# Kernel optimization log

Measured on AMD Instinct MI355X. Metric: run time of the kernel, lower is better.

The kernel has to match this reference:

```python
import jax, jax.numpy as jnp
import numpy as np
from jax import lax

B, C, L = 2048, 9605, 8
WL_PER_LABEL = 50
ALPHA = 0.5        # training_config['alpha4']
ALPHA1 = 0.1       # margin
ALPHA2 = 2.0       # training_config['alpha2']
ALPHA3 = 10.0      # training_config['alpha3']
ALPHA_OTHER = 0.5
NEG = jnp.float32(-1e30)


def setup_inputs() -> dict:
    key = jax.random.key(0)
    k1, k2, k3, k4 = jax.random.split(key, 4)
    x = jax.random.normal(k1, (B, C), dtype=jnp.float32) * 2.0
    y = (jax.random.uniform(k2, (B, C)) < 0.005).astype(jnp.float32)
    y_neg = (jax.random.uniform(k3, (B, C)) < 0.005).astype(jnp.float32)
    # whitelist masks: L app-labels, each whitelisting ~WL_PER_LABEL raw classes
    idx = jax.random.randint(k4, (L, WL_PER_LABEL), 0, C)
    wl_masks = jnp.zeros((L, C), dtype=bool).at[jnp.arange(L)[:, None], idx].set(True)
    return {"x": x, "y": y, "y_neg": y_neg, "wl_masks": wl_masks}


def reference(x, y, y_neg, wl_masks):
    # y_neg is consumed by the original forward (find_gt_whitelist) but never
    # affects the returned loss, faithfully ignored here.
    xs_pos = jax.nn.sigmoid(x)                                  # [B, C]
    # top_k_thres = max(11th-largest sigmoid, alpha_other)
    thres = jnp.maximum(lax.top_k(xs_pos, 11)[0][:, 10], ALPHA_OTHER)  # [B]
    # per-label whitelist max: m[b,l] = max_{c in wl_l} xs_pos[b,c]
    m = jnp.max(jnp.where(wl_masks[None, :, :], xs_pos[:, None, :], NEG), axis=-1)  # [B, L]
    # label l is a ground-truth whitelist label iff y has any positive in wl_l
    has_pos = jnp.einsum('bc,lc->bl', y, wl_masks.astype(y.dtype)) > 0   # [B, L]
    correct_max = jnp.max(jnp.where(has_pos, m, NEG), axis=-1)           # [B]
    incorrect_max = jnp.max(jnp.where(~has_pos, m, NEG), axis=-1)        # [B]
    any_correct = jnp.any(has_pos, axis=-1)
    any_incorrect = jnp.any(~has_pos, axis=-1)
    # union whitelist max (the "other" branch uses xs_pos over all wl indices)
    union_max = jnp.max(jnp.where(jnp.any(wl_masks, axis=0)[None, :], xs_pos, NEG), axis=-1)
    x1 = jnp.where(any_correct, correct_max, thres)
    x2 = jnp.where(any_correct,
                   jnp.where(any_incorrect, jnp.maximum(incorrect_max, thres), thres),
                   union_max)
    coef = jnp.where(any_correct, 1.0, 1.0 - ALPHA)
    d = x2 - x1 + ALPHA1
    rank = jnp.where(d > 0, ALPHA2, 1.0) * jax.nn.sigmoid(ALPHA3 * d)
    return jnp.mean(coef * rank)
```

## Files before the change

### kernel.cpp

```cpp
#include <hip/hip_runtime.h>

#define CC 9605
#define BB 2048
#define LL 8
#define CAND_MAX 384
#define NEGF (-1e30f)

#define WS_PARTIALS_OFF 16384

__device__ __forceinline__ unsigned enc_f(float f) {
  unsigned u = __float_as_uint(f);
  return (u & 0x80000000u) ? ~u : (u | 0x80000000u);
}
__device__ __forceinline__ float dec_u(unsigned e) {
  unsigned u = (e & 0x80000000u) ? (e & 0x7fffffffu) : ~e;
  return __uint_as_float(u);
}
__device__ __forceinline__ float sigm(float z) {
  return 1.0f / (1.0f + __expf(-z));
}

__global__ void wl_sniff(const unsigned* __restrict__ wlw,
                         unsigned* __restrict__ wsu) {
  const int nwords = (LL * CC) / 4;
  const int stride = gridDim.x * blockDim.x;
  unsigned f = 0u;
  for (int j = blockIdx.x * blockDim.x + threadIdx.x; j < nwords; j += stride) {
    unsigned w = wlw[j];
#pragma unroll
    for (int k = 0; k < 4; ++k) {
      unsigned b = (w >> (8 * k)) & 255u;
      if (b == 1u)    { f |= 2u; if (k != 0) f |= 1u; }
      if (b == 0x3fu) { f |= 8u; if (k == 1) f |= 4u; }
    }
  }
#pragma unroll
  for (int off = 32; off >= 1; off >>= 1) f |= __shfl_xor(f, off, 64);
  if ((threadIdx.x & 63) == 0 && f) atomicOr(&wsu[1], f);
}

__global__ void wl_compact(const unsigned char* __restrict__ wl,
                           unsigned* __restrict__ wsu) {
  const int tid = threadIdx.x;
  const int lane = tid & 63;
  const int c = blockIdx.x * 256 + tid;
  const unsigned g = wsu[1];
  const int dt = (g & 1u) ? 0 : (g & 4u) ? 3 : (g & 2u) ? 1 : (g & 8u) ? 2 : 0;
  const int* wl32 = (const int*)wl;
  const float* wlf = (const float*)wl;
  const unsigned short* wlh = (const unsigned short*)wl;
  unsigned m = 0u;
  if (c < CC) {
#pragma unroll
    for (int l = 0; l < LL; ++l) {
      int j = l * CC + c;
      bool on;
      if (dt == 0) on = (wl[j] != 0);
      else if (dt == 1) on = (wl32[j] != 0);
      else if (dt == 2) on = (wlf[j] != 0.0f);
      else on = (wlh[j] != 0);
      if (on) m |= (1u << l);
    }
  }
  unsigned long long bal = __ballot(m != 0u);
  if (bal) {
    unsigned wcnt = (unsigned)__popcll(bal);
    unsigned basep = 0u;
    if (lane == 0) basep = atomicAdd(&wsu[0], wcnt);
    basep = __shfl(basep, 0, 64);
    if (m) {
      unsigned pos = basep + (unsigned)__popcll(bal & ((1ull << lane) - 1ull));
      if (pos < 2048u) wsu[4 + pos] = ((unsigned)c << 8) | m;
    }
  }
}

__global__ __launch_bounds__(256, 4) void loss_kernel(
    const float* __restrict__ x, const float* __restrict__ y,
    const unsigned* __restrict__ wsu, float* __restrict__ partials) {
  __shared__ __align__(16) unsigned sh_row[9608];
  __shared__ unsigned sh_cand[CAND_MAX];
  __shared__ unsigned sh_redM[4];
  __shared__ unsigned sh_redC[4];
  __shared__ unsigned sh_cnt;
  __shared__ unsigned sh_e11;
  __shared__ float sh_wl[4][10];

  const int tid = threadIdx.x;
  const int lane = tid & 63;
  const int wid = tid >> 6;
  const int b = blockIdx.x;
  const long long base = (long long)b * CC;

  const int soff = (4 - (b & 3)) & 3;
  const int ngroups = (CC - soff) >> 2;
  const int tailn = CC - soff - (ngroups << 2);
  const int m_extra = soff + tailn;
  const float4* vp = (const float4*)(x + base + soff);
  float4 t[10];
#pragma unroll
  for (int i = 0; i < 9; ++i) t[i] = vp[tid + (i << 8)];
  const int g9 = tid + (9 << 8);
  if (g9 < ngroups) t[9] = vp[g9];
  else { t[9].x = NEGF; t[9].y = NEGF; t[9].z = NEGF; t[9].w = NEGF; }
  float tailv = NEGF;
  int tailcol = 0;
  if (tid < m_extra) {
    tailcol = (tid < soff) ? tid : (soff + (ngroups << 2) + (tid - soff));
    tailv = x[base + tailcol];
  }

  const unsigned nu = wsu[0];
  const unsigned* ents = wsu + 4;
  unsigned ent0 = 0u, ent1 = 0u;
  float gx0 = NEGF, gy0 = 0.0f, gx1 = NEGF, gy1 = 0.0f;
  const bool h0 = (unsigned)tid < nu;
  const bool h1 = (unsigned)(tid + 256) < nu;
  if (h0) ent0 = ents[tid];
  if (h1) ent1 = ents[tid + 256];
  if (h0) { gx0 = x[base + (ent0 >> 8)]; gy0 = y[base + (ent0 >> 8)]; }
  if (h1) { gx1 = x[base + (ent1 >> 8)]; gy1 = y[base + (ent1 >> 8)]; }

  uint4* rv = (uint4*)sh_row;
  unsigned mx = 0u;
#pragma unroll
  for (int i = 0; i < 10; ++i) {
    int g = tid + (i << 8);
    uint4 e;
    e.x = enc_f(t[i].x); e.y = enc_f(t[i].y);
    e.z = enc_f(t[i].z); e.w = enc_f(t[i].w);
    if (i < 9 || g < ngroups) {
      mx = max(mx, max(max(e.x, e.y), max(e.z, e.w)));
      rv[g] = e;
    }
  }
  if (tid < m_extra) {
    unsigned e = enc_f(tailv);
    mx = max(mx, e);
    sh_row[(ngroups << 2) + tid] = e;
  }
  if (tid < 3) sh_row[9605 + tid] = 0u;
  if (tid == 0) sh_cnt = 0u;

#pragma unroll
  for (int off = 32; off >= 1; off >>= 1) mx = max(mx, __shfl_xor(mx, off, 64));
  if (lane == 0) sh_redM[wid] = mx;
  __syncthreads();
  const unsigned Emax =
      max(max(sh_redM[0], sh_redM[1]), max(sh_redM[2], sh_redM[3]));

  auto blk_count = [&](unsigned T) -> unsigned {
    unsigned cnt = 0u;
#pragma unroll
    for (int i = 0; i < 10; ++i) {
      int g = tid + (i << 8);
      if (g < 2402) {
        uint4 v = rv[g];
        cnt += (v.x >= T) + (v.y >= T) + (v.z >= T) + (v.w >= T);
      }
    }
#pragma unroll
    for (int off = 32; off >= 1; off >>= 1) cnt += __shfl_xor(cnt, off, 64);
    __syncthreads();
    if (lane == 0) sh_redC[wid] = cnt;
    __syncthreads();
    return sh_redC[0] + sh_redC[1] + sh_redC[2] + sh_redC[3];
  };

  unsigned E11 = 0u;
  bool done = false;
  unsigned lo = (Emax > (1u << 23)) ? (Emax - (1u << 23)) : 1u;
  unsigned hi = Emax + 1u;
  unsigned c = blk_count(lo);
  while (c < 11u && lo > 1u) {
    hi = lo;
    lo = (lo > (1u << 23)) ? (lo - (1u << 23)) : 1u;
    c = blk_count(lo);
  }
  while (c > CAND_MAX) {
    if (hi - lo <= 1u) { E11 = lo; done = true; break; }
    unsigned mid = lo + ((hi - lo) >> 1);
    unsigned cm = blk_count(mid);
    if (cm >= 11u) { lo = mid; c = cm; } else { hi = mid; }
  }

  if (!done) {
#pragma unroll
    for (int i = 0; i < 10; ++i) {
      int g = tid + (i << 8);
      uint4 v;
      if (g < 2402) v = rv[g];
      else { v.x = 0u; v.y = 0u; v.z = 0u; v.w = 0u; }
      unsigned vals[4] = {v.x, v.y, v.z, v.w};
#pragma unroll
      for (int k = 0; k < 4; ++k) {
        bool pr = (vals[k] >= lo);
        unsigned long long bal = __ballot(pr);
        if (bal) {
          unsigned wcnt = (unsigned)__popcll(bal);
          unsigned basep = 0u;
          if (lane == 0) basep = atomicAdd(&sh_cnt, wcnt);
          basep = __shfl(basep, 0, 64);
          if (pr) {
            unsigned posn =
                basep + (unsigned)__popcll(bal & ((1ull << lane) - 1ull));
            sh_cand[posn] = vals[k];
          }
        }
      }
    }
    __syncthreads();

    if (wid == 0) {
      unsigned v0[6];
#pragma unroll
      for (int j = 0; j < 6; ++j) {
        unsigned idx = (unsigned)lane + 64u * j;
        v0[j] = (idx < c) ? sh_cand[idx] : 0u;
      }
      unsigned ans = 0u;
      for (int r = 0; r < 11; ++r) {
        unsigned lmx = v0[0];
#pragma unroll
        for (int j = 1; j < 6; ++j) lmx = max(lmx, v0[j]);
        unsigned wm = lmx;
#pragma unroll
        for (int off = 32; off >= 1; off >>= 1)
          wm = max(wm, __shfl_xor(wm, off, 64));
        ans = wm;
        if (r < 10) {
          unsigned long long bal = __ballot(lmx == wm);
          int first = (int)__ffsll((long long)bal) - 1;
          if (lane == first) {
            bool rm = false;
#pragma unroll
            for (int j = 0; j < 6; ++j) {
              if (!rm && v0[j] == wm) { v0[j] = 0u; rm = true; }
            }
          }
        }
      }
      if (lane == 0) sh_e11 = ans;
    }
    __syncthreads();
    E11 = sh_e11;
  }

  float lm[8];
#pragma unroll
  for (int l = 0; l < 8; ++l) lm[l] = NEGF;
  unsigned pmask = 0u;
  if (h0) {
    unsigned mk = ent0 & 255u;
    pmask |= mk;
    if (gy0 > 0.0f) pmask |= (mk << 8);
#pragma unroll
    for (int l = 0; l < 8; ++l)
      if ((mk >> l) & 1u) lm[l] = fmaxf(lm[l], gx0);
  }
  if (h1) {
    unsigned mk = ent1 & 255u;
    pmask |= mk;
    if (gy1 > 0.0f) pmask |= (mk << 8);
#pragma unroll
    for (int l = 0; l < 8; ++l)
      if ((mk >> l) & 1u) lm[l] = fmaxf(lm[l], gx1);
  }
  for (unsigned e = (unsigned)tid + 512u; e < nu; e += 256u) {
    unsigned ent = ents[e];
    unsigned mk = ent & 255u;
    float xv = x[base + (ent >> 8)];
    float yv = y[base + (ent >> 8)];
    pmask |= mk;
    if (yv > 0.0f) pmask |= (mk << 8);
#pragma unroll
    for (int l = 0; l < 8; ++l)
      if ((mk >> l) & 1u) lm[l] = fmaxf(lm[l], xv);
  }
#pragma unroll
  for (int off = 32; off >= 1; off >>= 1) {
    pmask |= __shfl_xor(pmask, off, 64);
#pragma unroll
    for (int l = 0; l < 8; ++l) lm[l] = fmaxf(lm[l], __shfl_xor(lm[l], off, 64));
  }
  if (lane == 0) {
#pragma unroll
    for (int l = 0; l < 8; ++l) sh_wl[wid][l] = lm[l];
    sh_wl[wid][8] = __uint_as_float(pmask);
  }
  __syncthreads();

  if (tid == 0) {
    float LM[8];
    unsigned PM = 0u;
#pragma unroll
    for (int l = 0; l < 8; ++l) LM[l] = NEGF;
    for (int w = 0; w < 4; ++w) {
#pragma unroll
      for (int l = 0; l < 8; ++l) LM[l] = fmaxf(LM[l], sh_wl[w][l]);
      PM |= __float_as_uint(sh_wl[w][8]);
    }
    unsigned PR = PM & 255u, PO = (PM >> 8) & 255u;
    float thres = fmaxf(sigm(dec_u(E11)), 0.5f);
    float cmax = NEGF, imax = NEGF, umax = NEGF;
#pragma unroll
    for (int l = 0; l < 8; ++l) {
      if ((PR >> l) & 1u) {
        float ml = sigm(LM[l]);
        umax = fmaxf(umax, ml);
        if ((PO >> l) & 1u) cmax = fmaxf(cmax, ml);
        else imax = fmaxf(imax, ml);
      }
    }
    bool anyc = (PO != 0u);
    bool anyi = (PO != 255u);
    float x1 = anyc ? cmax : thres;
    float x2 = anyc ? (anyi ? fmaxf(imax, thres) : thres)
                    : ((nu > 0u) ? umax : NEGF);
    float coef = anyc ? 1.0f : 0.5f;
    float dd = x2 - x1 + 0.1f;
    float rank = ((dd > 0.0f) ? 2.0f : 1.0f) * sigm(10.0f * dd);
    partials[b] = coef * rank;
  }
}

__global__ void final_reduce(const float* __restrict__ partials,
                             float* __restrict__ out) {
  __shared__ float sh[4];
  const int tid = threadIdx.x;
  const int lane = tid & 63;
  const int wid = tid >> 6;
  float s = 0.0f;
  for (int i = tid; i < BB; i += 256) s += partials[i];
#pragma unroll
  for (int off = 32; off >= 1; off >>= 1) s += __shfl_xor(s, off, 64);
  if (lane == 0) sh[wid] = s;
  __syncthreads();
  if (tid == 0) out[0] = (sh[0] + sh[1] + sh[2] + sh[3]) * (1.0f / (float)BB);
}

extern "C" void kernel_launch(void* const* d_in, const int* in_sizes, int n_in,
                              void* d_out, int out_size, void* d_ws,
                              size_t ws_size, hipStream_t stream) {
  const float* x = (const float*)d_in[0];
  const float* y = (const float*)d_in[1];
  const unsigned char* wl = (const unsigned char*)d_in[3];
  float* out = (float*)d_out;
  unsigned* wsu = (unsigned*)d_ws;
  float* partials = (float*)((char*)d_ws + WS_PARTIALS_OFF);

  hipMemsetAsync(d_ws, 0, 16, stream);
  wl_sniff<<<64, 256, 0, stream>>>((const unsigned*)wl, wsu);
  wl_compact<<<(CC + 255) / 256, 256, 0, stream>>>(wl, wsu);
  loss_kernel<<<BB, 256, 0, stream>>>(x, y, wsu, partials);
  final_reduce<<<1, 256, 0, stream>>>(partials, out);
}
```

Baseline: 230.3 us.

## Keep encoded row in registers instead of LDS, compact candidates via wave scan

Drops the ~38KB shared-memory row buffer and keeps each thread's encoded values in registers, so the threshold-count passes read registers instead of LDS. Candidate compaction now does one wave prefix scan and one atomic per wave instead of a ballot and atomic per element. Launch bounds rise from 4 to 6 blocks per SM to use the occupancy freed by the smaller LDS footprint, which may increase register pressure or cause spills.

```diff
diff --git a/kernel.cpp b/kernel.cpp
--- a/kernel.cpp
+++ b/kernel.cpp
@@ -75,10 +75,9 @@
   }
 }
 
-__global__ __launch_bounds__(256, 4) void loss_kernel(
+__global__ __launch_bounds__(256, 6) void loss_kernel(
     const float* __restrict__ x, const float* __restrict__ y,
     const unsigned* __restrict__ wsu, float* __restrict__ partials) {
-  __shared__ __align__(16) unsigned sh_row[9608];
   __shared__ unsigned sh_cand[CAND_MAX];
   __shared__ unsigned sh_redM[4];
   __shared__ unsigned sh_redC[4];
@@ -101,12 +100,12 @@
 #pragma unroll
   for (int i = 0; i < 9; ++i) t[i] = vp[tid + (i << 8)];
   const int g9 = tid + (9 << 8);
-  if (g9 < ngroups) t[9] = vp[g9];
-  else { t[9].x = NEGF; t[9].y = NEGF; t[9].z = NEGF; t[9].w = NEGF; }
-  float tailv = NEGF;
-  int tailcol = 0;
-  if (tid < m_extra) {
-    tailcol = (tid < soff) ? tid : (soff + (ngroups << 2) + (tid - soff));
+  const bool v9 = (g9 < ngroups);
+  if (v9) t[9] = vp[g9];
+  float tailv = 0.0f;
+  const bool has_tail = (tid < m_extra);
+  if (has_tail) {
+    int tailcol = (tid < soff) ? tid : (soff + (ngroups << 2) + (tid - soff));
     tailv = x[base + tailcol];
   }
 
@@ -121,25 +120,23 @@
   if (h0) { gx0 = x[base + (ent0 >> 8)]; gy0 = y[base + (ent0 >> 8)]; }
   if (h1) { gx1 = x[base + (ent1 >> 8)]; gy1 = y[base + (ent1 >> 8)]; }
 
-  uint4* rv = (uint4*)sh_row;
+  uint4 u[10];
   unsigned mx = 0u;
 #pragma unroll
-  for (int i = 0; i < 10; ++i) {
-    int g = tid + (i << 8);
-    uint4 e;
-    e.x = enc_f(t[i].x); e.y = enc_f(t[i].y);
-    e.z = enc_f(t[i].z); e.w = enc_f(t[i].w);
-    if (i < 9 || g < ngroups) {
-      mx = max(mx, max(max(e.x, e.y), max(e.z, e.w)));
-      rv[g] = e;
-    }
-  }
-  if (tid < m_extra) {
-    unsigned e = enc_f(tailv);
-    mx = max(mx, e);
-    sh_row[(ngroups << 2) + tid] = e;
-  }
-  if (tid < 3) sh_row[9605 + tid] = 0u;
+  for (int i = 0; i < 9; ++i) {
+    u[i].x = enc_f(t[i].x); u[i].y = enc_f(t[i].y);
+    u[i].z = enc_f(t[i].z); u[i].w = enc_f(t[i].w);
+    mx = max(mx, max(max(u[i].x, u[i].y), max(u[i].z, u[i].w)));
+  }
+  if (v9) {
+    u[9].x = enc_f(t[9].x); u[9].y = enc_f(t[9].y);
+    u[9].z = enc_f(t[9].z); u[9].w = enc_f(t[9].w);
+    mx = max(mx, max(max(u[9].x, u[9].y), max(u[9].z, u[9].w)));
+  } else {
+    u[9].x = 0u; u[9].y = 0u; u[9].z = 0u; u[9].w = 0u;
+  }
+  unsigned et = 0u;
+  if (has_tail) { et = enc_f(tailv); mx = max(mx, et); }
   if (tid == 0) sh_cnt = 0u;
 
 #pragma unroll
@@ -153,12 +150,9 @@
     unsigned cnt = 0u;
 #pragma unroll
     for (int i = 0; i < 10; ++i) {
-      int g = tid + (i << 8);
-      if (g < 2402) {
-        uint4 v = rv[g];
-        cnt += (v.x >= T) + (v.y >= T) + (v.z >= T) + (v.w >= T);
-      }
-    }
+      cnt += (u[i].x >= T) + (u[i].y >= T) + (u[i].z >= T) + (u[i].w >= T);
+    }
+    cnt += (et >= T);
 #pragma unroll
     for (int off = 32; off >= 1; off >>= 1) cnt += __shfl_xor(cnt, off, 64);
     __syncthreads();
@@ -185,30 +179,31 @@
   }
 
   if (!done) {
+    unsigned nloc = 0u;
 #pragma unroll
     for (int i = 0; i < 10; ++i) {
-      int g = tid + (i << 8);
-      uint4 v;
-      if (g < 2402) v = rv[g];
-      else { v.x = 0u; v.y = 0u; v.z = 0u; v.w = 0u; }
-      unsigned vals[4] = {v.x, v.y, v.z, v.w};
-#pragma unroll
-      for (int k = 0; k < 4; ++k) {
-        bool pr = (vals[k] >= lo);
-        unsigned long long bal = __ballot(pr);
-        if (bal) {
-          unsigned wcnt = (unsigned)__popcll(bal);
-          unsigned basep = 0u;
-          if (lane == 0) basep = atomicAdd(&sh_cnt, wcnt);
-          basep = __shfl(basep, 0, 64);
-          if (pr) {
-            unsigned posn =
-                basep + (unsigned)__popcll(bal & ((1ull << lane) - 1ull));
-            sh_cand[posn] = vals[k];
-          }
-        }
-      }
-    }
+      nloc += (u[i].x >= lo) + (u[i].y >= lo) + (u[i].z >= lo) + (u[i].w >= lo);
+    }
+    nloc += (et >= lo);
+    unsigned scan = nloc;
+#pragma unroll
+    for (int off = 1; off < 64; off <<= 1) {
+      unsigned nn = __shfl_up(scan, off, 64);
+      if (lane >= off) scan += nn;
+    }
+    unsigned wtot = __shfl(scan, 63, 64);
+    unsigned basep = 0u;
+    if (lane == 0) basep = atomicAdd(&sh_cnt, wtot);
+    basep = __shfl(basep, 0, 64);
+    unsigned pos = basep + scan - nloc;
+#pragma unroll
+    for (int i = 0; i < 10; ++i) {
+      if (u[i].x >= lo) sh_cand[pos++] = u[i].x;
+      if (u[i].y >= lo) sh_cand[pos++] = u[i].y;
+      if (u[i].z >= lo) sh_cand[pos++] = u[i].z;
+      if (u[i].w >= lo) sh_cand[pos++] = u[i].w;
+    }
+    if (et >= lo) sh_cand[pos++] = et;
     __syncthreads();
 
     if (wid == 0) {
```

New measurement: 223.7 us. -2.9%, faster.
